# Performance work log

Measured on AMD Instinct MI355X. Metric: run time of the kernel, lower is better.

The kernel has to match this reference:

```python
import jax, jax.numpy as jnp
import numpy as np

T = 4096          # prefill tokens (single sequence)
HK = 16           # key heads
HV = 32           # value heads
DK = 128          # key head dim
DV = 128          # value head dim
K = 4             # causal conv kernel width
QKV = 2 * HK * DK + HV * DV  # 8192


def setup_inputs() -> dict:
    key = jax.random.key(0)
    k1, k2, k3, k4, k5, k6 = jax.random.split(key, 6)
    return {
        "mixed_qkv": jax.random.normal(k1, (T, QKV), dtype=jnp.float32),
        "a": jax.random.normal(k2, (T, HV), dtype=jnp.float32),
        "b": jax.random.normal(k3, (T, HV), dtype=jnp.float32),
        "conv_w": jax.random.normal(k4, (QKV, K), dtype=jnp.float32) * 0.2,
        "dt_bias": jax.random.normal(k5, (HV,), dtype=jnp.float32),
        "alog": jax.random.normal(k6, (HV,), dtype=jnp.float32),
    }


def _l2norm(x, eps=1e-6):
    return x * jax.lax.rsqrt(jnp.sum(x * x, axis=-1, keepdims=True) + eps)


def _forward(mixed_qkv, a, b, conv_w, dt_bias, alog):
    # --- causal depthwise conv1d (zero initial conv state) + SiLU ---
    xp = jnp.pad(mixed_qkv, ((K - 1, 0), (0, 0)))  # [T+K-1, QKV]
    y = sum(conv_w[None, :, j] * xp[j:j + T] for j in range(K))  # [T, QKV]
    x = jax.nn.silu(y)

    # --- split q/k/v ---
    q, k_, v = jnp.split(x, [HK * DK, 2 * HK * DK], axis=-1)
    q = q.reshape(T, HK, DK)
    k_ = k_.reshape(T, HK, DK)
    v = v.reshape(T, HV, DV)

    # use_qk_l2norm_in_kernel=True: L2-norm q,k; scale q by dk^-0.5
    q = _l2norm(q) * (DK ** -0.5)
    k_ = _l2norm(k_)

    # GQA: repeat key-head q/k to value-head count
    grp = HV // HK
    q = jnp.repeat(q, grp, axis=1)   # [T, HV, DK]
    k_ = jnp.repeat(k_, grp, axis=1)  # [T, HV, DK]

    # --- fused_gdn_gating ---
    g = -jnp.exp(alog)[None, :] * jax.nn.softplus(a + dt_bias[None, :])  # [T, HV]
    beta = jax.nn.sigmoid(b)                                             # [T, HV]

    # --- gated delta-rule recurrence (equiv. to chunk_gated_delta_rule) ---
    S0 = jnp.zeros((HV, DK, DV), dtype=mixed_qkv.dtype)

    def step(S, inp):
        qt, kt, vt, gt, bt = inp
        S = S * jnp.exp(gt)[:, None, None]                 # gated decay
        pred = jnp.einsum('hk,hkv->hv', kt, S)             # k^T S
        delta = (vt - pred) * bt[:, None]                  # beta-scaled error
        S = S + jnp.einsum('hk,hv->hkv', kt, delta)        # delta update
        o = jnp.einsum('hk,hkv->hv', qt, S)                # query readout
        return S, o

    _, out = jax.lax.scan(step, S0, (q, k_, v, g, beta))
    return out  # [T, HV, DV]


def reference(mixed_qkv, a, b, conv_w, dt_bias, alog):
    return _forward(mixed_qkv, a, b, conv_w, dt_bias, alog)
```

## Files before the change

### kernel.cpp

```cpp
#include <hip/hip_runtime.h>

#define T_LEN 4096
#define HKn   16
#define HVn   32
#define DKn   128
#define DVn   128
#define QKVn  8192
#define NCH   64
#define CS    64

typedef __attribute__((ext_vector_type(8))) short short8;
typedef __attribute__((ext_vector_type(4))) float f32x4;
typedef __attribute__((ext_vector_type(4))) unsigned u32x4;
typedef __attribute__((ext_vector_type(4))) unsigned short us4;

#define OFF_QSH  ((size_t)0)
#define OFF_QSL  ((size_t)16777216)
#define OFF_KSH  ((size_t)33554432)
#define OFF_KSL  ((size_t)50331648)
#define OFF_KTH  ((size_t)67108864)
#define OFF_KTL  ((size_t)83886080)
#define OFF_VA   ((size_t)100663296)
#define OFF_GBL  ((size_t)167772160)
#define OFF_G    ((size_t)168820736)
#define OFF_WH   ((size_t)169345024)
#define OFF_WL   ((size_t)202899456)
#define OFF_MH   ((size_t)236453888)
#define OFF_ML   ((size_t)253231104)

template <int CTRL>
__device__ __forceinline__ float dpp_add(float x) {
    int v = __builtin_amdgcn_update_dpp(0, __float_as_int(x), CTRL, 0xF, 0xF, true);
    return x + __int_as_float(v);
}
__device__ __forceinline__ float reduce32g(float x) {
    x = dpp_add<0x128>(x); x = dpp_add<0x124>(x);
    x = dpp_add<0x122>(x); x = dpp_add<0x121>(x);
    int v = __builtin_amdgcn_ds_swizzle(__float_as_int(x), 0x401F);
    return x + __int_as_float(v);
}
__device__ __forceinline__ unsigned short bf16rne(float f) {
    unsigned x = __float_as_uint(f);
    return (unsigned short)((x + 0x7FFFu + ((x >> 16) & 1u)) >> 16);
}
__device__ __forceinline__ float bf16tof(unsigned short h) {
    return __uint_as_float(((unsigned)h) << 16);
}
__device__ __forceinline__ void bsplit(float f, unsigned short& h, unsigned short& l) {
    h = bf16rne(f);
    l = bf16rne(f - bf16tof(h));
}
__device__ __forceinline__ unsigned packsplit(float f) {
    unsigned short h, l; bsplit(f, h, l);
    return ((unsigned)h << 16) | (unsigned)l;
}
__device__ __forceinline__ f32x4 MF(short8 a, short8 b, f32x4 c) {
    return __builtin_amdgcn_mfma_f32_16x16x32_bf16(a, b, c, 0, 0, 0);
}
__device__ __forceinline__ void unpack8(u32x4 x0, u32x4 x1, short8& hi, short8& lo) {
    union { u32x4 u; short8 s; } H, L;
    H.u[0] = __builtin_amdgcn_perm(x0.y, x0.x, 0x07060302u);
    L.u[0] = __builtin_amdgcn_perm(x0.y, x0.x, 0x05040100u);
    H.u[1] = __builtin_amdgcn_perm(x0.w, x0.z, 0x07060302u);
    L.u[1] = __builtin_amdgcn_perm(x0.w, x0.z, 0x05040100u);
    H.u[2] = __builtin_amdgcn_perm(x1.y, x1.x, 0x07060302u);
    L.u[2] = __builtin_amdgcn_perm(x1.y, x1.x, 0x05040100u);
    H.u[3] = __builtin_amdgcn_perm(x1.w, x1.z, 0x07060302u);
    L.u[3] = __builtin_amdgcn_perm(x1.w, x1.z, 0x05040100u);
    hi = H.s; lo = L.s;
}
#define SB0() __builtin_amdgcn_sched_barrier(0)
#define BARL() do { \
    asm volatile("s_waitcnt lgkmcnt(0)" ::: "memory"); \
    __builtin_amdgcn_s_barrier(); \
    asm volatile("" ::: "memory"); \
} while (0)
#define WAITV0() do { \
    asm volatile("s_waitcnt vmcnt(0)" ::: "memory"); \
    SB0(); \
} while (0)
#define WAITL0() do { \
    asm volatile("s_waitcnt lgkmcnt(0)" ::: "memory"); \
    SB0(); \
} while (0)

typedef __attribute__((address_space(3))) void lds_t;
typedef const __attribute__((address_space(1))) void gbl_t;
__device__ __forceinline__ void load_lds16(const void* g, void* l) {
    __builtin_amdgcn_global_load_lds((gbl_t*)g, (lds_t*)l, 16, 0, 0);
}
__device__ __forceinline__ void load_lds4(const void* g, void* l) {
    __builtin_amdgcn_global_load_lds((gbl_t*)g, (lds_t*)l, 4, 0, 0);
}

__global__ __launch_bounds__(256) void k_gate(
    const float* __restrict__ a, const float* __restrict__ b,
    const float* __restrict__ dt_bias, const float* __restrict__ alog,
    float2* __restrict__ gbl)
{
    const int i = blockIdx.x * 256 + threadIdx.x;
    if (i < T_LEN * HVn) {
        const int h = i >> 12, t = i & (T_LEN - 1);
        const float av = a[(size_t)t * HVn + h];
        const float bv = b[(size_t)t * HVn + h];
        const float xv = av + dt_bias[h];
        const float sp = fmaxf(xv, 0.f) + log1pf(expf(-fabsf(xv)));
        const float g  = -expf(alog[h]) * sp;
        const float beta = 1.f / (1.f + expf(-bv));
        gbl[(size_t)h * T_LEN + t] = make_float2(beta, g);
    }
}

__global__ __launch_bounds__(128) void k_conv(
    const float* __restrict__ x, const float* __restrict__ w,
    const float* __restrict__ bgate,
    unsigned short* __restrict__ qsh, unsigned short* __restrict__ qsl,
    unsigned short* __restrict__ ksh, unsigned short* __restrict__ ksl,
    float* __restrict__ va2)
{
    const int t = blockIdx.x, seg = blockIdx.y, tid = threadIdx.x;
    const int c0 = seg * 512 + tid * 4;

    f32x4 wv[4];
    #pragma unroll
    for (int j = 0; j < 4; ++j) wv[j] = *(const f32x4*)(w + (size_t)(c0 + j) * 4);

    f32x4 acc;
    if (t >= 3) {
        const float* xb = x + (size_t)(t - 3) * QKVn + c0;
        const f32x4 x0 = *(const f32x4*)(xb);
        const f32x4 x1 = *(const f32x4*)(xb + QKVn);
        const f32x4 x2 = *(const f32x4*)(xb + 2 * QKVn);
        const f32x4 x3 = *(const f32x4*)(xb + 3 * QKVn);
        #pragma unroll
        for (int j = 0; j < 4; ++j)
            acc[j] = fmaf(wv[j][0], x0[j], fmaf(wv[j][1], x1[j],
                     fmaf(wv[j][2], x2[j], wv[j][3] * x3[j])));
    } else {
        f32x4 xs[4];
        #pragma unroll
        for (int p = 0; p < 4; ++p) {
            const int tt = t - 3 + p;
            if (tt >= 0) xs[p] = *(const f32x4*)(x + (size_t)tt * QKVn + c0);
            else         xs[p] = (f32x4){0.f, 0.f, 0.f, 0.f};
        }
        #pragma unroll
        for (int j = 0; j < 4; ++j)
            acc[j] = fmaf(wv[j][0], xs[0][j], fmaf(wv[j][1], xs[1][j],
                     fmaf(wv[j][2], xs[2][j], wv[j][3] * xs[3][j])));
    }
    f32x4 y;
    #pragma unroll
    for (int j = 0; j < 4; ++j) y[j] = acc[j] / (1.f + expf(-acc[j]));

    if (seg < 8) {
        float ss = y[0]*y[0] + y[1]*y[1] + y[2]*y[2] + y[3]*y[3];
        ss = reduce32g(ss);
        float r = rsqrtf(ss + 1e-6f);
        if (seg < 4) r *= 0.08838834764831845f;
        us4 hi, lo;
        #pragma unroll
        for (int j = 0; j < 4; ++j) {
            unsigned short hh, ll; bsplit(y[j] * r, hh, ll);
            hi[j] = hh; lo[j] = ll;
        }
        const int d = c0 & 127;
        if (seg < 4) {
            const int head = c0 >> 7;
            const size_t idx = ((size_t)head * T_LEN + t) * DKn + d;
            *(us4*)(qsh + idx) = hi; *(us4*)(qsl + idx) = lo;
        } else {
            const int head = (c0 - 2048) >> 7;
            const size_t idx = ((size_t)head * T_LEN + t) * DKn + d;
            *(us4*)(ksh + idx) = hi; *(us4*)(ksl + idx) = lo;
        }
    } else {
        const int h = (c0 - 4096) >> 7;
        const float bv = bgate[(size_t)t * HVn + h];
        const float beta = 1.f / (1.f + expf(-bv));
        f32x4 o;
        #pragma unroll
        for (int j = 0; j < 4; ++j) o[j] = y[j] * beta;
        *(f32x4*)(va2 + ((size_t)h * T_LEN + t) * DVn + (c0 & 127)) = o;
    }
}

__global__ __launch_bounds__(256) void k_tr(
    const unsigned short* __restrict__ ksh, const unsigned short* __restrict__ ksl,
    unsigned short* __restrict__ kth, unsigned short* __restrict__ ktl)
{
    __shared__ unsigned pk[64][65];
    const int b = blockIdx.x;
    const int kh = b >> 7, tt = (b >> 1) & 63, hh = b & 1;
    const int t0 = tt * 64, d0 = hh * 64;
    const int tid = threadIdx.x;
    #pragma unroll
    for (int e = 0; e < 16; ++e) {
        const int lin = e * 256 + tid;
        const int tl = lin >> 6, dl = lin & 63;
        const size_t o = ((size_t)kh * T_LEN + t0 + tl) * DKn + d0 + dl;
        pk[tl][dl] = ((unsigned)ksh[o] << 16) | (unsigned)ksl[o];
    }
    __syncthreads();
    #pragma unroll
    for (int e = 0; e < 16; ++e) {
        const int lin = e * 256 + tid;
        const int dl = lin >> 6, tl = lin & 63;
        const unsigned v = pk[tl][dl];
        const size_t o = ((size_t)kh * DKn + d0 + dl) * T_LEN + t0 + tl;
        kth[o] = (unsigned short)(v >> 16);
        ktl[o] = (unsigned short)(v & 0xFFFF);
    }
}

__global__ __launch_bounds__(256) void k_p1(
    const float2* __restrict__ gbl,
    const unsigned short* __restrict__ qsh, const unsigned short* __restrict__ qsl,
    const unsigned short* __restrict__ ksh, const unsigned short* __restrict__ ksl,
    float* __restrict__ va2, float* __restrict__ Gbuf,
    unsigned short* __restrict__ Wh, unsigned short* __restrict__ Wl,
    unsigned short* __restrict__ Mh, unsigned short* __restrict__ Ml)
{
    __shared__ float sA[64][68];
    __shared__ float sG[64];
    __shared__ float sB[64];
    const int blk = blockIdx.x;
    const int h = blk >> 6, ch = blk & 63;
    const int kh = h >> 1, t0 = ch * 64;
    const int tid = threadIdx.x, lane = tid & 63, wid = tid >> 6;
    const int l15 = lane & 15, lg = lane >> 4;

    if (tid < 64) {
        float2 g2 = gbl[(size_t)h * T_LEN + t0 + tid];
        sB[tid] = g2.x;
        float G = g2.y;
        #pragma unroll
        for (int s = 1; s < 64; s <<= 1) {
            float y = __int_as_float(__builtin_amdgcn_ds_bpermute((tid - s) << 2, __float_as_int(G)));
            G += (tid >= s) ? y : 0.f;
        }
        sG[tid] = G;
        Gbuf[(size_t)h * T_LEN + t0 + tid] = G;
    }
    __syncthreads();

    const char TIa[10] = {0,1,1,2,2,2,3,3,3,3};
    const char TJa[10] = {0,0,1,0,1,2,0,1,2,3};
    const size_t kbase = ((size_t)kh * T_LEN + t0) * DKn;
    for (int idx = wid; idx < 10; idx += 4) {
        const int mi = TIa[idx], nj = TJa[idx];
        f32x4 aKK = {0.f,0.f,0.f,0.f}, aQK = {0.f,0.f,0.f,0.f};
        #pragma unroll
        for (int kk = 0; kk < 4; ++kk) {
            const size_t offA = kbase + (size_t)(16*mi + l15) * DKn + 32*kk + 8*lg;
            const size_t offB = kbase + (size_t)(16*nj + l15) * DKn + 32*kk + 8*lg;
            short8 kAh = *(const short8*)(ksh + offA);
            short8 kAl = *(const short8*)(ksl + offA);
            short8 kBh = *(const short8*)(ksh + offB);
            short8 kBl = *(const short8*)(ksl + offB);
            short8 qAh = *(const short8*)(qsh + offA);
            short8 qAl = *(const short8*)(qsl + offA);
            aKK = MF(kAh,kBh,aKK); aKK = MF(kAh,kBl,aKK); aKK = MF(kAl,kBh,aKK);
            aQK = MF(qAh,kBh,aQK); aQK = MF(qAh,kBl,aQK); aQK = MF(qAl,kBh,aQK);
        }
        #pragma unroll
        for (int r = 0; r < 4; ++r) {
            const int i = 16*mi + 4*lg + r;
            const int j = 16*nj + l15;
            const float e = __expf(fminf(sG[i] - sG[j], 0.f));
            sA[i][j] = (j < i) ? sB[i] * e * aKK[r] : 0.f;
            const float mv = (j <= i) ? e * aQK[r] : 0.f;
            unsigned short mh, ml; bsplit(mv, mh, ml);
            const size_t moff = (((size_t)h * NCH + ch) * CS + i) * CS + j;
            Mh[moff] = mh; Ml[moff] = ml;
        }
    }
    __syncthreads();

    const int c = tid;
    float X[64];
    if (c < 128) {
        #pragma unroll
        for (int i = 0; i < 64; ++i)
            X[i] = va2[((size_t)h * T_LEN + t0 + i) * DVn + c];
    } else {
        const int dk = c - 128;
        #pragma unroll
        for (int i = 0; i < 64; ++i) {
            const size_t o = ((size_t)kh * T_LEN + t0 + i) * DKn + dk;
            const float kf = bf16tof(ksh[o]) + bf16tof(ksl[o]);
            X[i] = sB[i] * __expf(sG[i]) * kf;
        }
    }
    #pragma unroll
    for (int i = 1; i < 64; ++i) {
        float acc = X[i];
        const int nq = (i + 3) >> 2;
        #pragma unroll
        for (int q = 0; q < nq; ++q) {
            const f32x4 aa = *(const f32x4*)&sA[i][4*q];
            acc = fmaf(-aa[0], X[4*q+0], acc);
            acc = fmaf(-aa[1], X[4*q+1], acc);
            acc = fmaf(-aa[2], X[4*q+2], acc);
            acc = fmaf(-aa[3], X[4*q+3], acc);
        }
        X[i] = acc;
    }
    if (c < 128) {
        #pragma unroll
        for (int i = 0; i < 64; ++i)
            va2[((size_t)h * T_LEN + t0 + i) * DVn + c] = X[i];
    } else {
        const int dk = c - 128;
        #pragma unroll
        for (int i = 0; i < 64; ++i) {
            unsigned short wh, wl; bsplit(-X[i], wh, wl);
            const size_t o = (((size_t)h * NCH + ch) * CS + i) * DKn + dk;
            Wh[o] = wh; Wl[o] = wl;
        }
    }
}

#define SLOT  1024
#define OFF_GROW 28672
#define OFF_U    28928
#define WSTG  29952

__global__ __launch_bounds__(256, 1) void k_p2(
    const unsigned short* __restrict__ qsh, const unsigned short* __restrict__ qsl,
    const unsigned short* __restrict__ kth, const unsigned short* __restrict__ ktl,
    const unsigned short* __restrict__ Wh, const unsigned short* __restrict__ Wl,
    const unsigned short* __restrict__ Mh, const unsigned short* __restrict__ Ml,
    const float* __restrict__ va2, const float* __restrict__ Gbuf,
    float* __restrict__ out)
{
    __shared__ __align__(16) char stg[4][WSTG];
    __shared__ unsigned sSp[16][132];
    __shared__ unsigned sDLp[16][68];
    __shared__ unsigned sDSp[16][68];

    const int p = blockIdx.x;
    const int slot = p >> 3;
    const int h  = (p & 7) * 4 + (slot & 3);
    const int nb = slot >> 2;
    const int kh = h >> 1, n0 = nb * 16;
    const int tid = threadIdx.x, lane = tid & 63, wid = tid >> 6;
    const int l15 = lane & 15, lg = lane >> 4;

    char* wb = &stg[wid][0];

    short8 Sbh[4], Sbl[4];
    f32x4 Sc[2];
    const short8 z8 = {0,0,0,0,0,0,0,0};
    #pragma unroll
    for (int kk = 0; kk < 4; ++kk) { Sbh[kk] = z8; Sbl[kk] = z8; }
    Sc[0] = (f32x4){0.f,0.f,0.f,0.f};
    Sc[1] = (f32x4){0.f,0.f,0.f,0.f};

    auto stage_ch = [&](int ch) {
        const int t0 = ch * CS;
        const size_t wbase = (((size_t)h * NCH + ch) * CS + 16*wid + l15) * DKn + 8*lg;
        #pragma unroll
        for (int kk = 0; kk < 4; ++kk) {
            load_lds16(Wh + wbase + 32*kk, wb + (0 + kk) * SLOT);
            load_lds16(Wl + wbase + 32*kk, wb + (4 + kk) * SLOT);
        }
        const size_t kb0 = ((size_t)kh * DKn + 16*wid + l15) * T_LEN + t0 + 8*lg;
        const size_t kb1 = ((size_t)kh * DKn + 16*(wid + 4) + l15) * T_LEN + t0 + 8*lg;
        #pragma unroll
        for (int k2 = 0; k2 < 2; ++k2) {
            load_lds16(kth + kb0 + 32*k2, wb + (8  + k2) * SLOT);
            load_lds16(kth + kb1 + 32*k2, wb + (10 + k2) * SLOT);
            load_lds16(ktl + kb0 + 32*k2, wb + (12 + k2) * SLOT);
            load_lds16(ktl + kb1 + 32*k2, wb + (14 + k2) * SLOT);
        }
        const size_t qbase = ((size_t)kh * T_LEN + t0 + 16*wid + l15) * DKn + 8*lg;
        #pragma unroll
        for (int kk = 0; kk < 4; ++kk) {
            load_lds16(qsh + qbase + 32*kk, wb + (16 + kk) * SLOT);
            load_lds16(qsl + qbase + 32*kk, wb + (20 + kk) * SLOT);
        }
        const size_t mbase = (((size_t)h * NCH + ch) * CS + 16*wid + l15) * CS + 8*lg;
        #pragma unroll
        for (int k2 = 0; k2 < 2; ++k2) {
            load_lds16(Mh + mbase + 32*k2, wb + (24 + k2) * SLOT);
            load_lds16(Ml + mbase + 32*k2, wb + (26 + k2) * SLOT);
        }
        load_lds4(Gbuf + (size_t)h * T_LEN + t0 + lane, wb + OFF_GROW);
        #pragma unroll
        for (int r = 0; r < 4; ++r)
            load_lds4(va2 + ((size_t)h * T_LEN + t0 + 16*wid + 4*lg + r) * DVn + n0 + l15,
                      wb + OFF_U + r * 256);
    };

    stage_ch(0);

    #pragma unroll 1
    for (int ch = 0; ch < NCH; ++ch) {
        const int t0 = ch * CS;
        WAITV0();

        const float* gw = (const float*)(wb + OFF_GROW);
        float gr[4];
        #pragma unroll
        for (int r = 0; r < 4; ++r) gr[r] = gw[16*wid + 4*lg + r];
        const float g63 = gw[63];
        const float lam = __expf(g63);
        float scE[4], eg[4];
        #pragma unroll
        for (int r = 0; r < 4; ++r) { scE[r] = __expf(g63 - gr[r]); eg[r] = __expf(gr[r]); }
        float uf[4];
        #pragma unroll
        for (int r = 0; r < 4; ++r) uf[r] = *(const float*)(wb + OFF_U + r * 256 + lane * 4);

        f32x4 d0 = {uf[0], uf[1], uf[2], uf[3]};
        f32x4 d1 = {0.f,0.f,0.f,0.f}, d2 = {0.f,0.f,0.f,0.f};
        #pragma unroll
        for (int kk = 0; kk < 4; ++kk) {
            const short8 wh8 = *(const short8*)(wb + (0 + kk) * SLOT + lane * 16);
            const short8 wl8 = *(const short8*)(wb + (4 + kk) * SLOT + lane * 16);
            d0 = MF(wh8, Sbh[kk], d0);
            d1 = MF(wh8, Sbl[kk], d1);
            d2 = MF(wl8, Sbh[kk], d2);
        }
        f32x4 dl;
        #pragma unroll
        for (int r = 0; r < 4; ++r) dl[r] = d0[r] + d1[r] + d2[r];

        const int cc0 = 16*wid + 4*lg;
        u32x4 pdl, pds;
        #pragma unroll
        for (int r = 0; r < 4; ++r) {
            pdl[r] = packsplit(dl[r]);
            pds[r] = packsplit(dl[r] * scE[r]);
        }
        *(u32x4*)&sDLp[l15][cc0] = pdl;
        *(u32x4*)&sDSp[l15][cc0] = pds;
        BARL();

        short8 dlh[2], dll[2], dsh[2], dsl[2];
        #pragma unroll
        for (int k2 = 0; k2 < 2; ++k2) {
            u32x4 x0 = *(const u32x4*)&sDLp[l15][32*k2 + 8*lg];
            u32x4 x1 = *(const u32x4*)&sDLp[l15][32*k2 + 8*lg + 4];
            unpack8(x0, x1, dlh[k2], dll[k2]);
            u32x4 y0 = *(const u32x4*)&sDSp[l15][32*k2 + 8*lg];
            u32x4 y1 = *(const u32x4*)&sDSp[l15][32*k2 + 8*lg + 4];
            unpack8(y0, y1, dsh[k2], dsl[k2]);
        }

        #pragma unroll
        for (int m2 = 0; m2 < 2; ++m2) {
            f32x4 t0a = {0.f,0.f,0.f,0.f}, t1a = {0.f,0.f,0.f,0.f}, t2a = {0.f,0.f,0.f,0.f};
            #pragma unroll
            for (int k2 = 0; k2 < 2; ++k2) {
                const short8 th8 = *(const short8*)(wb + (8 + 2*m2 + k2) * SLOT + lane * 16);
                const short8 tl8 = *(const short8*)(wb + (12 + 2*m2 + k2) * SLOT + lane * 16);
                t0a = MF(th8, dsh[k2], t0a);
                t1a = MF(th8, dsl[k2], t1a);
                t2a = MF(tl8, dsh[k2], t2a);
            }
            u32x4 ps;
            #pragma unroll
            for (int r = 0; r < 4; ++r) {
                Sc[m2][r] = fmaf(lam, Sc[m2][r], t0a[r] + t1a[r] + t2a[r]);
                ps[r] = packsplit(Sc[m2][r]);
            }
            *(u32x4*)&sSp[l15][16*wid + 64*m2 + 4*lg] = ps;
        }
        BARL();

        f32x4 aq = {0.f,0.f,0.f,0.f}, am = {0.f,0.f,0.f,0.f};
        #pragma unroll
        for (int kk = 0; kk < 4; ++kk) {
            const short8 qh8 = *(const short8*)(wb + (16 + kk) * SLOT + lane * 16);
            const short8 ql8 = *(const short8*)(wb + (20 + kk) * SLOT + lane * 16);
            aq = MF(qh8, Sbh[kk], aq); aq = MF(qh8, Sbl[kk], aq); aq = MF(ql8, Sbh[kk], aq);
        }
        #pragma unroll
        for (int k2 = 0; k2 < 2; ++k2) {
            const short8 mh8 = *(const short8*)(wb + (24 + k2) * SLOT + lane * 16);
            const short8 ml8 = *(const short8*)(wb + (26 + k2) * SLOT + lane * 16);
            am = MF(mh8, dlh[k2], am); am = MF(mh8, dll[k2], am); am = MF(ml8, dlh[k2], am);
        }
        #pragma unroll
        for (int r = 0; r < 4; ++r) {
            const int cc = cc0 + r;
            out[((size_t)(t0 + cc) * HVn + h) * DVn + n0 + l15] = fmaf(eg[r], aq[r], am[r]);
        }

        if (ch + 1 < NCH) {
            WAITL0();
            stage_ch(ch + 1);
        }

        #pragma unroll
        for (int kk = 0; kk < 4; ++kk) {
            u32x4 z0 = *(const u32x4*)&sSp[l15][32*kk + 8*lg];
            u32x4 z1 = *(const u32x4*)&sSp[l15][32*kk + 8*lg + 4];
            unpack8(z0, z1, Sbh[kk], Sbl[kk]);
        }
    }
}

extern "C" void kernel_launch(void* const* d_in, const int* in_sizes, int n_in,
                              void* d_out, int out_size, void* d_ws, size_t ws_size,
                              hipStream_t stream) {
    const float* mixed_qkv = (const float*)d_in[0];
    const float* a         = (const float*)d_in[1];
    const float* b         = (const float*)d_in[2];
    const float* conv_w    = (const float*)d_in[3];
    const float* dt_bias   = (const float*)d_in[4];
    const float* alog      = (const float*)d_in[5];
    float* out = (float*)d_out;
    char* ws = (char*)d_ws;

    unsigned short* qsh = (unsigned short*)(ws + OFF_QSH);
    unsigned short* qsl = (unsigned short*)(ws + OFF_QSL);
    unsigned short* ksh = (unsigned short*)(ws + OFF_KSH);
    unsigned short* ksl = (unsigned short*)(ws + OFF_KSL);
    unsigned short* kth = (unsigned short*)(ws + OFF_KTH);
    unsigned short* ktl = (unsigned short*)(ws + OFF_KTL);
    float*  va2 = (float*)(ws + OFF_VA);
    float2* gbl = (float2*)(ws + OFF_GBL);
    float*  Gbf = (float*)(ws + OFF_G);
    unsigned short* Wh = (unsigned short*)(ws + OFF_WH);
    unsigned short* Wl = (unsigned short*)(ws + OFF_WL);
    unsigned short* Mh = (unsigned short*)(ws + OFF_MH);
    unsigned short* Ml = (unsigned short*)(ws + OFF_ML);

    k_gate<<<(T_LEN * HVn + 255) / 256, 256, 0, stream>>>(a, b, dt_bias, alog, gbl);

    dim3 cgrid(T_LEN, 16);
    k_conv<<<cgrid, 128, 0, stream>>>(mixed_qkv, conv_w, b, qsh, qsl, ksh, ksl, va2);

    k_tr<<<2048, 256, 0, stream>>>(ksh, ksl, kth, ktl);

    k_p1<<<HVn * NCH, 256, 0, stream>>>(gbl, qsh, qsl, ksh, ksl, va2, Gbf, Wh, Wl, Mh, Ml);

    k_p2<<<HVn * 8, 256, 0, stream>>>(qsh, qsl, kth, ktl, Wh, Wl, Mh, Ml, va2, Gbf, out);
}
```

Baseline: 556.2 us.

## Collapse k_p2 to a single wave per block with double-buffered staging

The recurrence kernel k_p2 now runs one 64-lane wave per block instead of four waves. That one wave handles all four 16-row subtiles of each chunk, which removes the s_barrier synchronisations between the delta, state-update and output phases. Chunk staging is double-buffered in LDS so the next chunk's W/K/u/g loads overlap the current chunk's output computation. Q and M fragments are now read straight from global memory into registers. In exchange each block does four times the serial MFMA work per chunk and uses many more registers, so per-chunk latency on the sequential critical path may grow.

```diff
diff --git a/kernel.cpp b/kernel.cpp
--- a/kernel.cpp
+++ b/kernel.cpp
@@ -70,11 +70,6 @@
     hi = H.s; lo = L.s;
 }
 #define SB0() __builtin_amdgcn_sched_barrier(0)
-#define BARL() do { \
-    asm volatile("s_waitcnt lgkmcnt(0)" ::: "memory"); \
-    __builtin_amdgcn_s_barrier(); \
-    asm volatile("" ::: "memory"); \
-} while (0)
 #define WAITV0() do { \
     asm volatile("s_waitcnt vmcnt(0)" ::: "memory"); \
     SB0(); \
@@ -321,12 +316,14 @@
     }
 }
 
-#define SLOT  1024
-#define OFF_GROW 28672
-#define OFF_U    28928
-#define WSTG  29952
-
-__global__ __launch_bounds__(256, 1) void k_p2(
+#define SLOTB  1024
+#define WS_W   0
+#define WS_KT  32768
+#define WS_U   65536
+#define WS_G   69632
+#define BUFSZ  69888
+
+__global__ __launch_bounds__(64, 1) void k_p2(
     const unsigned short* __restrict__ qsh, const unsigned short* __restrict__ qsl,
     const unsigned short* __restrict__ kth, const unsigned short* __restrict__ ktl,
     const unsigned short* __restrict__ Wh, const unsigned short* __restrict__ Wl,
@@ -334,128 +331,115 @@
     const float* __restrict__ va2, const float* __restrict__ Gbuf,
     float* __restrict__ out)
 {
-    __shared__ __align__(16) char stg[4][WSTG];
-    __shared__ unsigned sSp[16][132];
-    __shared__ unsigned sDLp[16][68];
-    __shared__ unsigned sDSp[16][68];
+    __shared__ __align__(16) char stg[2][BUFSZ];
+    __shared__ unsigned exDL[16][68];
+    __shared__ unsigned exDS[16][68];
+    __shared__ unsigned exS [16][132];
 
     const int p = blockIdx.x;
     const int slot = p >> 3;
     const int h  = (p & 7) * 4 + (slot & 3);
-    const int nb = slot >> 2;
-    const int kh = h >> 1, n0 = nb * 16;
-    const int tid = threadIdx.x, lane = tid & 63, wid = tid >> 6;
+    const int cs = slot >> 2;
+    const int kh = h >> 1, n0 = cs * 16;
+    const int lane = threadIdx.x & 63;
     const int l15 = lane & 15, lg = lane >> 4;
 
-    char* wb = &stg[wid][0];
+    auto stage_ch = [&](int ch, char* wb) {
+        const int t0s = ch * CS;
+        #pragma unroll
+        for (int mi = 0; mi < 4; ++mi)
+            #pragma unroll
+            for (int kk = 0; kk < 4; ++kk) {
+                const size_t g = (((size_t)h * NCH + ch) * CS + 16*mi + l15) * DKn + 32*kk + 8*lg;
+                load_lds16(Wh + g, wb + WS_W + (mi*4 + kk) * SLOTB);
+                load_lds16(Wl + g, wb + WS_W + (16 + mi*4 + kk) * SLOTB);
+            }
+        #pragma unroll
+        for (int mi2 = 0; mi2 < 8; ++mi2)
+            #pragma unroll
+            for (int k2 = 0; k2 < 2; ++k2) {
+                const size_t g = ((size_t)kh * DKn + 16*mi2 + l15) * T_LEN + t0s + 32*k2 + 8*lg;
+                load_lds16(kth + g, wb + WS_KT + (mi2*2 + k2) * SLOTB);
+                load_lds16(ktl + g, wb + WS_KT + (16 + mi2*2 + k2) * SLOTB);
+            }
+        #pragma unroll
+        for (int mi = 0; mi < 4; ++mi)
+            #pragma unroll
+            for (int r = 0; r < 4; ++r)
+                load_lds4(va2 + ((size_t)h * T_LEN + t0s + 16*mi + 4*lg + r) * DVn + n0 + l15,
+                          wb + WS_U + (mi*4 + r) * 256);
+        load_lds4(Gbuf + (size_t)h * T_LEN + t0s + lane, wb + WS_G);
+    };
 
     short8 Sbh[4], Sbl[4];
-    f32x4 Sc[2];
+    f32x4 Sc[8];
     const short8 z8 = {0,0,0,0,0,0,0,0};
     #pragma unroll
     for (int kk = 0; kk < 4; ++kk) { Sbh[kk] = z8; Sbl[kk] = z8; }
-    Sc[0] = (f32x4){0.f,0.f,0.f,0.f};
-    Sc[1] = (f32x4){0.f,0.f,0.f,0.f};
-
-    auto stage_ch = [&](int ch) {
-        const int t0 = ch * CS;
-        const size_t wbase = (((size_t)h * NCH + ch) * CS + 16*wid + l15) * DKn + 8*lg;
-        #pragma unroll
-        for (int kk = 0; kk < 4; ++kk) {
-            load_lds16(Wh + wbase + 32*kk, wb + (0 + kk) * SLOT);
-            load_lds16(Wl + wbase + 32*kk, wb + (4 + kk) * SLOT);
-        }
-        const size_t kb0 = ((size_t)kh * DKn + 16*wid + l15) * T_LEN + t0 + 8*lg;
-        const size_t kb1 = ((size_t)kh * DKn + 16*(wid + 4) + l15) * T_LEN + t0 + 8*lg;
-        #pragma unroll
-        for (int k2 = 0; k2 < 2; ++k2) {
-            load_lds16(kth + kb0 + 32*k2, wb + (8  + k2) * SLOT);
-            load_lds16(kth + kb1 + 32*k2, wb + (10 + k2) * SLOT);
-            load_lds16(ktl + kb0 + 32*k2, wb + (12 + k2) * SLOT);
-            load_lds16(ktl + kb1 + 32*k2, wb + (14 + k2) * SLOT);
-        }
-        const size_t qbase = ((size_t)kh * T_LEN + t0 + 16*wid + l15) * DKn + 8*lg;
-        #pragma unroll
-        for (int kk = 0; kk < 4; ++kk) {
-            load_lds16(qsh + qbase + 32*kk, wb + (16 + kk) * SLOT);
-            load_lds16(qsl + qbase + 32*kk, wb + (20 + kk) * SLOT);
-        }
-        const size_t mbase = (((size_t)h * NCH + ch) * CS + 16*wid + l15) * CS + 8*lg;
-        #pragma unroll
-        for (int k2 = 0; k2 < 2; ++k2) {
-            load_lds16(Mh + mbase + 32*k2, wb + (24 + k2) * SLOT);
-            load_lds16(Ml + mbase + 32*k2, wb + (26 + k2) * SLOT);
-        }
-        load_lds4(Gbuf + (size_t)h * T_LEN + t0 + lane, wb + OFF_GROW);
-        #pragma unroll
-        for (int r = 0; r < 4; ++r)
-            load_lds4(va2 + ((size_t)h * T_LEN + t0 + 16*wid + 4*lg + r) * DVn + n0 + l15,
-                      wb + OFF_U + r * 256);
-    };
-
-    stage_ch(0);
+    #pragma unroll
+    for (int mi = 0; mi < 8; ++mi) Sc[mi] = (f32x4){0.f,0.f,0.f,0.f};
+
+    stage_ch(0, &stg[0][0]);
+    int cur = 0;
 
     #pragma unroll 1
     for (int ch = 0; ch < NCH; ++ch) {
         const int t0 = ch * CS;
         WAITV0();
-
-        const float* gw = (const float*)(wb + OFF_GROW);
-        float gr[4];
-        #pragma unroll
-        for (int r = 0; r < 4; ++r) gr[r] = gw[16*wid + 4*lg + r];
+        const char* wb = &stg[cur][0];
+        const float* gw = (const float*)(wb + WS_G);
         const float g63 = gw[63];
         const float lam = __expf(g63);
-        float scE[4], eg[4];
-        #pragma unroll
-        for (int r = 0; r < 4; ++r) { scE[r] = __expf(g63 - gr[r]); eg[r] = __expf(gr[r]); }
-        float uf[4];
-        #pragma unroll
-        for (int r = 0; r < 4; ++r) uf[r] = *(const float*)(wb + OFF_U + r * 256 + lane * 4);
-
-        f32x4 d0 = {uf[0], uf[1], uf[2], uf[3]};
-        f32x4 d1 = {0.f,0.f,0.f,0.f}, d2 = {0.f,0.f,0.f,0.f};
-        #pragma unroll
-        for (int kk = 0; kk < 4; ++kk) {
-            const short8 wh8 = *(const short8*)(wb + (0 + kk) * SLOT + lane * 16);
-            const short8 wl8 = *(const short8*)(wb + (4 + kk) * SLOT + lane * 16);
-            d0 = MF(wh8, Sbh[kk], d0);
-            d1 = MF(wh8, Sbl[kk], d1);
-            d2 = MF(wl8, Sbh[kk], d2);
-        }
-        f32x4 dl;
-        #pragma unroll
-        for (int r = 0; r < 4; ++r) dl[r] = d0[r] + d1[r] + d2[r];
-
-        const int cc0 = 16*wid + 4*lg;
-        u32x4 pdl, pds;
-        #pragma unroll
-        for (int r = 0; r < 4; ++r) {
-            pdl[r] = packsplit(dl[r]);
-            pds[r] = packsplit(dl[r] * scE[r]);
-        }
-        *(u32x4*)&sDLp[l15][cc0] = pdl;
-        *(u32x4*)&sDSp[l15][cc0] = pds;
-        BARL();
+
+        f32x4 dl[4];
+        #pragma unroll
+        for (int mi = 0; mi < 4; ++mi) {
+            f32x4 d0, d1 = {0.f,0.f,0.f,0.f}, d2 = {0.f,0.f,0.f,0.f};
+            #pragma unroll
+            for (int r = 0; r < 4; ++r)
+                d0[r] = *(const float*)(wb + WS_U + (mi*4 + r) * 256 + lane * 4);
+            #pragma unroll
+            for (int kk = 0; kk < 4; ++kk) {
+                const short8 wh8 = *(const short8*)(wb + WS_W + (mi*4 + kk) * SLOTB + lane * 16);
+                const short8 wl8 = *(const short8*)(wb + WS_W + (16 + mi*4 + kk) * SLOTB + lane * 16);
+                d0 = MF(wh8, Sbh[kk], d0);
+                d1 = MF(wh8, Sbl[kk], d1);
+                d2 = MF(wl8, Sbh[kk], d2);
+            }
+            #pragma unroll
+            for (int r = 0; r < 4; ++r) dl[mi][r] = d0[r] + d1[r] + d2[r];
+        }
+        #pragma unroll
+        for (int mi = 0; mi < 4; ++mi) {
+            u32x4 pdl, pds;
+            #pragma unroll
+            for (int r = 0; r < 4; ++r) {
+                pdl[r] = packsplit(dl[mi][r]);
+                pds[r] = packsplit(dl[mi][r] * __expf(g63 - gw[16*mi + 4*lg + r]));
+            }
+            *(u32x4*)&exDL[l15][16*mi + 4*lg] = pdl;
+            *(u32x4*)&exDS[l15][16*mi + 4*lg] = pds;
+        }
+        WAITL0();
 
         short8 dlh[2], dll[2], dsh[2], dsl[2];
         #pragma unroll
         for (int k2 = 0; k2 < 2; ++k2) {
-            u32x4 x0 = *(const u32x4*)&sDLp[l15][32*k2 + 8*lg];
-            u32x4 x1 = *(const u32x4*)&sDLp[l15][32*k2 + 8*lg + 4];
+            u32x4 x0 = *(const u32x4*)&exDL[l15][32*k2 + 8*lg];
+            u32x4 x1 = *(const u32x4*)&exDL[l15][32*k2 + 8*lg + 4];
             unpack8(x0, x1, dlh[k2], dll[k2]);
-            u32x4 y0 = *(const u32x4*)&sDSp[l15][32*k2 + 8*lg];
-            u32x4 y1 = *(const u32x4*)&sDSp[l15][32*k2 + 8*lg + 4];
+            u32x4 y0 = *(const u32x4*)&exDS[l15][32*k2 + 8*lg];
+            u32x4 y1 = *(const u32x4*)&exDS[l15][32*k2 + 8*lg + 4];
             unpack8(y0, y1, dsh[k2], dsl[k2]);
         }
 
         #pragma unroll
-        for (int m2 = 0; m2 < 2; ++m2) {
+        for (int mi2 = 0; mi2 < 8; ++mi2) {
             f32x4 t0a = {0.f,0.f,0.f,0.f}, t1a = {0.f,0.f,0.f,0.f}, t2a = {0.f,0.f,0.f,0.f};
             #pragma unroll
             for (int k2 = 0; k2 < 2; ++k2) {
-                const short8 th8 = *(const short8*)(wb + (8 + 2*m2 + k2) * SLOT + lane * 16);
-                const short8 tl8 = *(const short8*)(wb + (12 + 2*m2 + k2) * SLOT + lane * 16);
+                const short8 th8 = *(const short8*)(wb + WS_KT + (mi2*2 + k2) * SLOTB + lane * 16);
+                const short8 tl8 = *(const short8*)(wb + WS_KT + (16 + mi2*2 + k2) * SLOTB + lane * 16);
                 t0a = MF(th8, dsh[k2], t0a);
                 t1a = MF(th8, dsl[k2], t1a);
                 t2a = MF(tl8, dsh[k2], t2a);
@@ -463,43 +447,65 @@
             u32x4 ps;
             #pragma unroll
             for (int r = 0; r < 4; ++r) {
-                Sc[m2][r] = fmaf(lam, Sc[m2][r], t0a[r] + t1a[r] + t2a[r]);
-                ps[r] = packsplit(Sc[m2][r]);
-            }
-            *(u32x4*)&sSp[l15][16*wid + 64*m2 + 4*lg] = ps;
-        }
-        BARL();
-
-        f32x4 aq = {0.f,0.f,0.f,0.f}, am = {0.f,0.f,0.f,0.f};
+                Sc[mi2][r] = fmaf(lam, Sc[mi2][r], t0a[r] + t1a[r] + t2a[r]);
+                ps[r] = packsplit(Sc[mi2][r]);
+            }
+            *(u32x4*)&exS[l15][16*mi2 + 4*lg] = ps;
+        }
+
+        short8 qfh[4][4], qfl[4][4], mfh[4][2], mfl[4][2];
+        #pragma unroll
+        for (int mi = 0; mi < 4; ++mi) {
+            const size_t qb = ((size_t)kh * T_LEN + t0 + 16*mi + l15) * DKn;
+            #pragma unroll
+            for (int kk = 0; kk < 4; ++kk) {
+                qfh[mi][kk] = *(const short8*)(qsh + qb + 32*kk + 8*lg);
+                qfl[mi][kk] = *(const short8*)(qsl + qb + 32*kk + 8*lg);
+            }
+            const size_t mb = (((size_t)h * NCH + ch) * CS + 16*mi + l15) * CS;
+            #pragma unroll
+            for (int k2 = 0; k2 < 2; ++k2) {
+                mfh[mi][k2] = *(const short8*)(Mh + mb + 32*k2 + 8*lg);
+                mfl[mi][k2] = *(const short8*)(Ml + mb + 32*k2 + 8*lg);
+            }
+        }
+
+        if (ch + 1 < NCH) stage_ch(ch + 1, &stg[cur ^ 1][0]);
+
+        #pragma unroll
+        for (int mi = 0; mi < 4; ++mi) {
+            f32x4 a0 = {0.f,0.f,0.f,0.f}, a1 = {0.f,0.f,0.f,0.f}, a2 = {0.f,0.f,0.f,0.f};
+            f32x4 m0 = {0.f,0.f,0.f,0.f}, m1 = {0.f,0.f,0.f,0.f}, m2c = {0.f,0.f,0.f,0.f};
+            #pragma unroll
+            for (int kk = 0; kk < 4; ++kk) {
+                a0 = MF(qfh[mi][kk], Sbh[kk], a0);
+                a1 = MF(qfh[mi][kk], Sbl[kk], a1);
+                a2 = MF(qfl[mi][kk], Sbh[kk], a2);
+            }
+            #pragma unroll
+            for (int k2 = 0; k2 < 2; ++k2) {
+                m0 = MF(mfh[mi][k2], dlh[k2], m0);
+                m1 = MF(mfh[mi][k2], dll[k2], m1);
+                m2c = MF(mfl[mi][k2], dlh[k2], m2c);
+            }
+            #pragma unroll
+            for (int r = 0; r < 4; ++r) {
+                const int tt = t0 + 16*mi + 4*lg + r;
+                const float aq = a0[r] + a1[r] + a2[r];
+                const float am = m0[r] + m1[r] + m2c[r];
+                out[((size_t)tt * HVn + h) * DVn + n0 + l15] =
+                    fmaf(__expf(gw[16*mi + 4*lg + r]), aq, am);
+            }
+        }
+
+        WAITL0();
         #pragma unroll
         for (int kk = 0; kk < 4; ++kk) {
-            const short8 qh8 = *(const short8*)(wb + (16 + kk) * SLOT + lane * 16);
-            const short8 ql8 = *(const short8*)(wb + (20 + kk) * SLOT + lane * 16);
-            aq = MF(qh8, Sbh[kk], aq); aq = MF(qh8, Sbl[kk], aq); aq = MF(ql8, Sbh[kk], aq);
-        }
-        #pragma unroll
-        for (int k2 = 0; k2 < 2; ++k2) {
-            const short8 mh8 = *(const short8*)(wb + (24 + k2) * SLOT + lane * 16);
-            const short8 ml8 = *(const short8*)(wb + (26 + k2) * SLOT + lane * 16);
-            am = MF(mh8, dlh[k2], am); am = MF(mh8, dll[k2], am); am = MF(ml8, dlh[k2], am);
-        }
-        #pragma unroll
-        for (int r = 0; r < 4; ++r) {
-            const int cc = cc0 + r;
-            out[((size_t)(t0 + cc) * HVn + h) * DVn + n0 + l15] = fmaf(eg[r], aq[r], am[r]);
-        }
-
-        if (ch + 1 < NCH) {
-            WAITL0();
-            stage_ch(ch + 1);
-        }
-
-        #pragma unroll
-        for (int kk = 0; kk < 4; ++kk) {
-            u32x4 z0 = *(const u32x4*)&sSp[l15][32*kk + 8*lg];
-            u32x4 z1 = *(const u32x4*)&sSp[l15][32*kk + 8*lg + 4];
+            u32x4 z0 = *(const u32x4*)&exS[l15][32*kk + 8*lg];
+            u32x4 z1 = *(const u32x4*)&exS[l15][32*kk + 8*lg + 4];
             unpack8(z0, z1, Sbh[kk], Sbl[kk]);
         }
+        cur ^= 1;
     }
 }
 
@@ -538,5 +544,5 @@
 
     k_p1<<<HVn * NCH, 256, 0, stream>>>(gbl, qsh, qsl, ksh, ksl, va2, Gbf, Wh, Wl, Mh, Ml);
 
-    k_p2<<<HVn * 8, 256, 0, stream>>>(qsh, qsl, kth, ktl, Wh, Wl, Mh, Ml, va2, Gbf, out);
-}
+    k_p2<<<256, 64, 0, stream>>>(qsh, qsl, kth, ktl, Wh, Wl, Mh, Ml, va2, Gbf, out);
+}
```

Measured after the change: 723.9 us. +30.2%, slower.
